# Optimization experiments

Measured on AMD Instinct MI355X. Metric: run time of the kernel, lower is better.

## Reference

```python
import jax, jax.numpy as jnp
import numpy as np

OBS, ACT, NTRAIN, BATCH = 8, 4, 128, 8
DIN = OBS + ACT


def setup_inputs() -> dict:
    key = jax.random.key(0)
    ks = jax.random.split(key, 11)
    f32 = jnp.float32
    m_x = jax.random.normal(ks[0], (BATCH, OBS), dtype=f32)
    A = 0.1 * jax.random.normal(ks[1], (BATCH, OBS, OBS), dtype=f32)
    s_x = A @ jnp.swapaxes(A, -1, -2) + 0.01 * jnp.eye(OBS, dtype=f32)  # SPD obs covariance
    m_u = jax.random.normal(ks[2], (BATCH, ACT), dtype=f32)
    Au = 0.1 * jax.random.normal(ks[3], (BATCH, ACT, ACT), dtype=f32)
    s_u = Au @ jnp.swapaxes(Au, -1, -2) + 0.01 * jnp.eye(ACT, dtype=f32)
    c_xu = 0.05 * jax.random.normal(ks[4], (BATCH, OBS, ACT), dtype=f32)
    X_train = jax.random.normal(ks[5], (NTRAIN, DIN), dtype=f32)
    lengthscales = jax.random.uniform(ks[6], (OBS, DIN), dtype=f32, minval=0.5, maxval=2.0)
    variances = jax.random.uniform(ks[7], (OBS, 1), dtype=f32, minval=0.5, maxval=1.5)
    noises = jax.random.uniform(ks[8], (OBS,), dtype=f32, minval=0.01, maxval=0.1)
    R = jax.random.normal(ks[9], (OBS, NTRAIN, NTRAIN), dtype=f32) / np.float32(np.sqrt(NTRAIN))
    inv_K = R @ jnp.swapaxes(R, -1, -2) + 0.1 * jnp.eye(NTRAIN, dtype=f32)  # SPD like a true K^-1
    beta = 0.1 * jax.random.normal(ks[10], (OBS, NTRAIN), dtype=f32)
    return dict(m_x=m_x, s_x=s_x, m_u=m_u, s_u=s_u, c_xu=c_xu, X_train=X_train,
                lengthscales=lengthscales, variances=variances, noises=noises,
                inv_K=inv_K, beta=beta)


def _forward(m_x, s_x, m_u, s_u, c_xu, X_train, lengthscales, variances, noises, inv_K, beta):
    obs_dim, input_dim = lengthscales.shape
    n = X_train.shape[0]
    eyeD = jnp.eye(input_dim, dtype=m_x.dtype)
    # joint input distribution over [x, u]
    joint_mean = jnp.concatenate([m_x, m_u], axis=-1)                      # [B, D]
    s_ = s_x @ c_xu                                                        # [B, obs, act] (as in source)
    upper = jnp.concatenate([s_x, s_], axis=-1)                            # [B, obs, D]
    lower = jnp.concatenate([jnp.swapaxes(s_, -1, -2), s_u], axis=-1)      # [B, act, D]
    joint_var = jnp.concatenate([upper, lower], axis=-2)                   # [B, D, D]
    # --- predictive mean (moment matching) ---
    inp = X_train[None, :, :] - joint_mean[:, None, :]                     # [B, N, D]
    inv_ls = 1.0 / lengthscales                                            # [E, D]
    inv_N = inp[:, None, :, :] * inv_ls[None, :, None, :]                  # [B, E, N, D]
    B_mat = inv_ls[None, :, :, None] * joint_var[:, None, :, :] * inv_ls[None, :, None, :] + eyeD
    t = jnp.swapaxes(jnp.linalg.solve(B_mat, jnp.swapaxes(inv_N, -1, -2)), -1, -2)  # [B, E, N, D]
    scaled_exp = jnp.exp(-0.5 * jnp.sum(inv_N * t, axis=-1))               # [B, E, N]
    lb = scaled_exp * beta[None, :, :]                                     # [B, E, N]
    det_B = jnp.linalg.det(B_mat)                                          # [B, E]
    var_v = variances[:, 0]                                                # [E]
    c = var_v[None, :] / jnp.sqrt(det_B)                                   # [B, E]
    pred_mean = jnp.sum(lb, axis=-1) * c                                   # [B, E]
    # --- input-output cross covariance ---
    t_inv_L = t * inv_ls[None, :, None, :]                                 # [B, E, N, D]
    cross_cov = jnp.swapaxes(jnp.einsum('bend,ben->bed', t_inv_L, lb) * c[..., None], -1, -2)  # [B, D, E]
    # --- predictive covariance: vectorized over all (a, b) output pairs ---
    X_i = X_train[:, None, :]
    X_j = X_train[None, :, :]
    diff = X_i - X_j                                                       # [N, N, D]
    l2 = lengthscales ** 2
    inv_l2 = 1.0 / l2

    def pair(l2_a, inv_a, var_a, beta_a, l2_b, inv_b, var_b, beta_b):
        inv_sum = inv_a + inv_b                                            # [D]
        Lam = 1.0 / inv_sum
        z_bar = Lam * (X_i * inv_a + X_j * inv_b)                          # [N, N, D]
        z = z_bar[None, :, :, :] - joint_mean[:, None, None, :]            # [B, N, N, D]
        z_flat = z.reshape(z.shape[0], n * n, input_dim)
        R_ab = joint_var * inv_sum[None, None, :] + eyeD                   # joint_var @ diag(inv_sum) + I
        exp1 = -0.5 * jnp.sum(diff * diff * (1.0 / (l2_a + l2_b)), axis=-1)  # [N, N]
        M_ab = joint_var + jnp.diag(Lam)[None, :, :]                       # [B, D, D]
        solved = jnp.swapaxes(jnp.linalg.solve(M_ab, jnp.swapaxes(z_flat, -1, -2)), -1, -2)
        exp2 = (-0.5 * jnp.sum(z_flat * solved, axis=-1)).reshape(z.shape[0], n, n)
        c_ab = var_a * var_b / jnp.sqrt(jnp.linalg.det(R_ab))              # [B]
        Q = c_ab[:, None, None] * jnp.exp(exp1[None, :, :] + exp2)         # [B, N, N]
        main = jnp.einsum('i,bij,j->b', beta_a, Q, beta_b)                 # [B]
        return main, Q

    pair_b = jax.vmap(pair, in_axes=(None, None, None, None, 0, 0, 0, 0))
    pair_ab = jax.vmap(pair_b, in_axes=(0, 0, 0, 0, None, None, None, None))
    main, Q = pair_ab(l2, inv_l2, var_v, beta, l2, inv_l2, var_v, beta)    # [E, E, B], [E, E, B, N, N]
    pred_cov = jnp.moveaxis(main, -1, 0)                                   # [B, E, E]
    idx = jnp.arange(obs_dim)
    Q_diag = Q[idx, idx]                                                   # [E, B, N, N]
    trace_val = jnp.einsum('eij,ebji->eb', inv_K, Q_diag)                  # [E, B]
    diag_corr = var_v[:, None] - trace_val + noises[:, None]               # [E, B]
    pred_cov = pred_cov + diag_corr.T[:, :, None] * jnp.eye(obs_dim, dtype=m_x.dtype)
    pred_cov = pred_cov - pred_mean[:, :, None] * pred_mean[:, None, :]
    pred_cov = 0.5 * (pred_cov + jnp.swapaxes(pred_cov, -1, -2))
    # --- propagate state moments ---
    cov_xf = upper @ cross_cov                                             # [B, obs, obs]
    m_out = m_x + pred_mean
    s_out = s_x + pred_cov + cov_xf + jnp.swapaxes(cov_xf, -1, -2)
    s_out = 0.5 * (s_out + jnp.swapaxes(s_out, -1, -2)) + 1e-8 * jnp.eye(obs_dim, dtype=m_x.dtype)
    return m_out, s_out


def reference(m_x, s_x, m_u, s_u, c_xu, X_train, lengthscales, variances, noises, inv_K, beta):
    return _forward(m_x, s_x, m_u, s_u, c_xu, X_train, lengthscales, variances, noises, inv_K, beta)
```

## Files before the change

kernel.cpp:

```cpp
#include <hip/hip_runtime.h>
#include <math.h>

#define OBS 8
#define ACT 4
#define DIN 12
#define NTRAIN 128
#define BATCH 8
#define NPAIR 36
#define NPT (BATCH*NPAIR)
#define NGT (BATCH*OBS)
#define NTASK (NPT+NGT)
#define THREADS 512
#define HSTRIDE 16

#define WS_PM  0
#define WS_CC  64
#define WS_MN  832
#define WS_TR  1344

__global__ void __launch_bounds__(THREADS) k_fused(
    const float* __restrict__ m_x, const float* __restrict__ s_x,
    const float* __restrict__ m_u, const float* __restrict__ s_u,
    const float* __restrict__ c_xu, const float* __restrict__ X,
    const float* __restrict__ ls, const float* __restrict__ vars,
    const float* __restrict__ beta, const float* __restrict__ invK,
    float* __restrict__ ws)
{
    int blk = blockIdx.x, tid = threadIdx.x;
    int lane = tid & 63, w = tid >> 6;
    bool isPair = blk < NPT;
    int b, a = 0, c = 0, e = 0;
    if (isPair) {
        b = blk / NPAIR;
        int rem = blk % NPAIR;
        while (rem >= OBS - a) { rem -= OBS - a; a++; }
        c = a + rem;
    } else {
        int q = blk - NPT; b = q / OBS; e = q % OBS;
    }

    __shared__ float jvs[144];
    __shared__ float Wl[144];
    __shared__ float mu[DIN];
    __shared__ float sc_wsum[DIN], sc_iA[DIN], sc_qc[DIN], sc_lam[DIN], sc_isum[DIN];
    __shared__ float s_cab;
    __shared__ __align__(16) float h[NTRAIN][HSTRIDE];
    __shared__ __align__(16) float2 bw[NTRAIN];
    __shared__ float red[8][13];

    int j0 = 2*lane;
    float xa[12], xb[12], xi[12];
    {
        const float4* xr = (const float4*)(X + j0*DIN);
        float4 t0 = xr[0], t1 = xr[1], t2 = xr[2], t3 = xr[3], t4 = xr[4], t5 = xr[5];
        xa[0]=t0.x; xa[1]=t0.y; xa[2]=t0.z; xa[3]=t0.w;
        xa[4]=t1.x; xa[5]=t1.y; xa[6]=t1.z; xa[7]=t1.w;
        xa[8]=t2.x; xa[9]=t2.y; xa[10]=t2.z; xa[11]=t2.w;
        xb[0]=t3.x; xb[1]=t3.y; xb[2]=t3.z; xb[3]=t3.w;
        xb[4]=t4.x; xb[5]=t4.y; xb[6]=t4.z; xb[7]=t4.w;
        xb[8]=t5.x; xb[9]=t5.y; xb[10]=t5.z; xb[11]=t5.w;
    }
    if (tid < NTRAIN) {
        const float4* xr = (const float4*)(X + tid*DIN);
        float4 t0 = xr[0], t1 = xr[1], t2 = xr[2];
        xi[0]=t0.x; xi[1]=t0.y; xi[2]=t0.z; xi[3]=t0.w;
        xi[4]=t1.x; xi[5]=t1.y; xi[6]=t1.z; xi[7]=t1.w;
        xi[8]=t2.x; xi[9]=t2.y; xi[10]=t2.z; xi[11]=t2.w;
    }

    if (tid < 144) {
        int r = tid / 12, cl = tid % 12;
        float v;
        if (r < OBS && cl < OBS) {
            v = s_x[(b*OBS+r)*OBS + cl];
        } else if (r < OBS) {
            v = 0.f;
            #pragma unroll
            for (int k = 0; k < OBS; k++)
                v += s_x[(b*OBS+r)*OBS+k] * c_xu[(b*OBS+k)*ACT + (cl-OBS)];
        } else if (cl < OBS) {
            v = 0.f;
            #pragma unroll
            for (int k = 0; k < OBS; k++)
                v += s_x[(b*OBS+cl)*OBS+k] * c_xu[(b*OBS+k)*ACT + (r-OBS)];
        } else {
            v = s_u[(b*ACT+r-OBS)*ACT + (cl-OBS)];
        }
        jvs[tid] = v;
    } else if (tid >= 160 && tid < 172) {
        int d = tid - 160;
        mu[d] = (d < OBS) ? m_x[b*OBS+d] : m_u[b*ACT+d-OBS];
    } else if (tid >= 192 && tid < 204) {
        int d = tid - 192;
        if (isPair) {
            float la = ls[a*DIN+d]; la *= la;
            float lc = ls[c*DIN+d]; lc *= lc;
            float ia = 1.f/la, ic = 1.f/lc;
            float is = ia + ic;
            float L  = 1.f/is;
            sc_wsum[d] = 1.f/(la+lc);
            sc_iA[d] = L*ia;
            sc_qc[d] = L*ic;
            sc_lam[d] = L;
            sc_isum[d] = is;
        } else {
            sc_iA[d] = 1.f / ls[e*DIN+d];
        }
    }
    __syncthreads();

    if (tid < DIN) {
        int r = tid;
        float row[12];
        if (isPair) {
            #pragma unroll
            for (int j = 0; j < 12; j++) row[j] = jvs[r*12+j];
            row[r] += sc_lam[r];
        } else {
            float ir = sc_iA[r];
            #pragma unroll
            for (int j = 0; j < 12; j++) row[j] = ir * sc_iA[j] * jvs[r*12+j];
            row[r] += 1.f;
        }
        float det = 1.f;
        #pragma unroll
        for (int k = 0; k < 12; k++) {
            float p = __shfl(row[k], k);
            float ip = 1.f / p;
            det *= p;
            float prow[12];
            #pragma unroll
            for (int j = 0; j < 12; j++) prow[j] = __shfl(row[j], k) * ip;
            if (r == k) {
                #pragma unroll
                for (int j = 0; j < 12; j++) row[j] = prow[j];
                row[k] = ip;
            } else {
                float f = row[k];
                #pragma unroll
                for (int j = 0; j < 12; j++) if (j != k) row[j] -= f * prow[j];
                row[k] = -f * ip;
            }
        }
        #pragma unroll
        for (int j = 0; j < 12; j++) Wl[r*12+j] = row[j];
        if (r == 0) {
            if (isPair) {
                float s = det;
                #pragma unroll
                for (int d = 0; d < 12; d++) s *= sc_isum[d];
                s_cab = vars[a]*vars[c] / sqrtf(s);
            } else {
                s_cab = vars[e] / sqrtf(det);
            }
        }
    }
    __syncthreads();

    if (isPair) {
        bool diag = (a == c);
        if (tid < NTRAIN) {
            int t = tid;
            float r[12], q[12]; float e1 = 0.f;
            #pragma unroll
            for (int d = 0; d < 12; d++) {
                r[d] = sc_iA[d]*xi[d] - mu[d];
                q[d] = sc_qc[d]*xi[d];
                e1 += sc_wsum[d]*xi[d]*xi[d];
            }
            float hrow[16];
            float alpha = 0.f, bq = 0.f;
            #pragma unroll
            for (int d = 0; d < 12; d++) {
                float u = 0.f, uq = 0.f;
                #pragma unroll
                for (int cl = 0; cl < 12; cl++) {
                    float wv = Wl[d*12+cl];
                    u  += wv*r[cl];
                    uq += wv*q[cl];
                }
                alpha += r[d]*u;
                bq    += q[d]*uq;
                hrow[d] = sc_wsum[d]*xi[d] - u*sc_qc[d];
            }
            hrow[12] = -0.5f*(e1 + alpha);
            hrow[13] = beta[a*NTRAIN+t];
            hrow[14] = 0.f; hrow[15] = 0.f;
            float4* hp = (float4*)&h[t][0];
            hp[0] = make_float4(hrow[0],hrow[1],hrow[2],hrow[3]);
            hp[1] = make_float4(hrow[4],hrow[5],hrow[6],hrow[7]);
            hp[2] = make_float4(hrow[8],hrow[9],hrow[10],hrow[11]);
            hp[3] = make_float4(hrow[12],hrow[13],hrow[14],hrow[15]);
            bw[t] = make_float2(-0.5f*(e1 + bq), beta[c*NTRAIN+t]);
        }
        __syncthreads();
        float4 bwv = ((const float4*)bw)[lane];
        float basej0 = bwv.x, wc0 = bwv.y, basej1 = bwv.z, wc1 = bwv.w;
        float am0 = 0.f, am1 = 0.f, at0 = 0.f, at1 = 0.f;
        const float2* Kb = (const float2*)(invK + a*NTRAIN*NTRAIN);
        #pragma unroll 4
        for (int k = 0; k < 16; k++) {
            int i = w + 8*k;
            const float4* hp = (const float4*)&h[i][0];
            float4 h0 = hp[0], h1 = hp[1], h2 = hp[2];
            float2 h3 = *(const float2*)&h[i][12];
            float sA0 = fmaf(h0.x,xa[0], fmaf(h0.y,xa[1], fmaf(h0.z,xa[2], h0.w*xa[3])));
            float sB0 = fmaf(h1.x,xa[4], fmaf(h1.y,xa[5], fmaf(h1.z,xa[6], h1.w*xa[7])));
            float sC0 = fmaf(h2.x,xa[8], fmaf(h2.y,xa[9], fmaf(h2.z,xa[10], h2.w*xa[11])));
            float sA1 = fmaf(h0.x,xb[0], fmaf(h0.y,xb[1], fmaf(h0.z,xb[2], h0.w*xb[3])));
            float sB1 = fmaf(h1.x,xb[4], fmaf(h1.y,xb[5], fmaf(h1.z,xb[6], h1.w*xb[7])));
            float sC1 = fmaf(h2.x,xb[8], fmaf(h2.y,xb[9], fmaf(h2.z,xb[10], h2.w*xb[11])));
            float e0  = __expf(sA0 + sB0 + sC0 + h3.x + basej0);
            float e1v = __expf(sA1 + sB1 + sC1 + h3.x + basej1);
            am0 = fmaf(h3.y, e0, am0);
            am1 = fmaf(h3.y, e1v, am1);
            if (diag) {
                float2 kv = Kb[i*64 + lane];
                at0 = fmaf(kv.x, e0, at0);
                at1 = fmaf(kv.y, e1v, at1);
            }
        }
        float accm = am0*wc0 + am1*wc1;
        float acct = at0 + at1;
        #pragma unroll
        for (int off = 32; off >= 1; off >>= 1) {
            accm += __shfl_xor(accm, off, 64);
            acct += __shfl_xor(acct, off, 64);
        }
        if (lane == 0) { red[w][0] = accm; red[w][1] = acct; }
        __syncthreads();
        if (tid == 0) {
            float m = 0.f, t = 0.f;
            #pragma unroll
            for (int v = 0; v < 8; v++) { m += red[v][0]; t += red[v][1]; }
            m *= s_cab; t *= s_cab;
            ws[WS_MN + b*64 + a*8 + c] = m;
            ws[WS_MN + b*64 + c*8 + a] = m;
            if (diag) ws[WS_TR + b*8 + a] = t;
        }
    } else {
        float vals[13];
        #pragma unroll
        for (int v = 0; v < 13; v++) vals[v] = 0.f;
        if (tid < NTRAIN) {
            int n = tid;
            float iN[12];
            #pragma unroll
            for (int d = 0; d < 12; d++) iN[d] = (xi[d]-mu[d]) * sc_iA[d];
            float qq = 0.f; float tv[12];
            #pragma unroll
            for (int d = 0; d < 12; d++) {
                float u = 0.f;
                #pragma unroll
                for (int cl = 0; cl < 12; cl++) u += Wl[d*12+cl]*iN[cl];
                tv[d] = u; qq += iN[d]*u;
            }
            float lb = __expf(-0.5f*qq) * beta[e*NTRAIN+n];
            vals[0] = lb;
            #pragma unroll
            for (int d = 0; d < 12; d++) vals[1+d] = tv[d]*sc_iA[d]*lb;
        }
        #pragma unroll
        for (int v = 0; v < 13; v++)
            #pragma unroll
            for (int off = 32; off >= 1; off >>= 1) vals[v] += __shfl_xor(vals[v], off, 64);
        if (lane == 0) {
            #pragma unroll
            for (int v = 0; v < 13; v++) red[w][v] = vals[v];
        }
        __syncthreads();
        if (tid == 0) {
            float cn = s_cab;
            ws[WS_PM + b*OBS + e] = cn*(red[0][0]+red[1][0]);
            for (int d = 0; d < 12; d++)
                ws[WS_CC + (b*DIN+d)*OBS + e] = cn*(red[0][1+d]+red[1][1+d]);
        }
    }
}

__global__ void k_final(const float* __restrict__ m_x, const float* __restrict__ s_x,
                        const float* __restrict__ c_xu, const float* __restrict__ vars,
                        const float* __restrict__ noises, const float* __restrict__ ws,
                        float* __restrict__ out) {
    int b = blockIdx.x, t = threadIdx.x;
    __shared__ float pm[OBS];
    __shared__ float sxs[64];
    const float* cc = ws + WS_CC + b*DIN*OBS;
    const float* mn = ws + WS_MN + b*64;
    const float* tr = ws + WS_TR + b*OBS;
    sxs[t] = s_x[b*64 + t];
    if (t < OBS) {
        float p = ws[WS_PM + b*OBS + t];
        pm[t] = p;
        out[b*OBS + t] = m_x[b*OBS + t] + p;
    }
    __syncthreads();
    int r = t >> 3, cl = t & 7;
    float P = mn[r*8 + cl];
    if (r == cl) P += vars[r] - tr[r] + noises[r];
    P -= pm[r]*pm[cl];
    float cxf = 0.f, cxfT = 0.f;
    #pragma unroll
    for (int d = 0; d < 8; d++) {
        cxf  += sxs[r*8+d]  * cc[d*8+cl];
        cxfT += sxs[cl*8+d] * cc[d*8+r];
    }
    #pragma unroll
    for (int d = 0; d < 4; d++) {
        float jr = 0.f, jc = 0.f;
        #pragma unroll
        for (int k = 0; k < 8; k++) {
            float cx = c_xu[(b*OBS+k)*ACT + d];
            jr += sxs[r*8+k]  * cx;
            jc += sxs[cl*8+k] * cx;
        }
        cxf  += jr * cc[(8+d)*8 + cl];
        cxfT += jc * cc[(8+d)*8 + r];
    }
    float S = sxs[r*8+cl] + P + cxf + cxfT;
    if (r == cl) S += 1e-8f;
    out[64 + b*64 + t] = S;
}

extern "C" void kernel_launch(void* const* d_in, const int* in_sizes, int n_in,
                              void* d_out, int out_size, void* d_ws, size_t ws_size,
                              hipStream_t stream) {
    const float* m_x    = (const float*)d_in[0];
    const float* s_x    = (const float*)d_in[1];
    const float* m_u    = (const float*)d_in[2];
    const float* s_u    = (const float*)d_in[3];
    const float* c_xu   = (const float*)d_in[4];
    const float* X      = (const float*)d_in[5];
    const float* ls     = (const float*)d_in[6];
    const float* vars   = (const float*)d_in[7];
    const float* noises = (const float*)d_in[8];
    const float* invK   = (const float*)d_in[9];
    const float* beta   = (const float*)d_in[10];
    float* out = (float*)d_out;
    float* ws  = (float*)d_ws;

    k_fused<<<NTASK, THREADS, 0, stream>>>(m_x, s_x, m_u, s_u, c_xu, X, ls, vars,
                                           beta, invK, ws);
    k_final<<<BATCH, 64, 0, stream>>>(m_x, s_x, c_xu, vars, noises, ws, out);
}
```

Baseline: 91.38 us.

## Merge GP-mean tasks into diagonal pair blocks and fuse final epilogue via last-block atomic

Folds the per-output GP mean/cross-covariance work into the diagonal pair blocks. It runs that work on threads 128-255 alongside the h-row setup, with both 12x12 inversions done in parallel in one wavefront. The separate finalization kernel is replaced by a last-block-done pattern: an atomic counter in the workspace, reset by a memset each launch, picks one block to compute the epilogue. This removes 64 extra blocks and one kernel launch, at the cost of an added memset, a device-wide atomic with fences, and a serialized tail in the last block.

```diff
diff --git a/kernel.cpp b/kernel.cpp
--- a/kernel.cpp
+++ b/kernel.cpp
@@ -7,9 +7,7 @@
 #define NTRAIN 128
 #define BATCH 8
 #define NPAIR 36
-#define NPT (BATCH*NPAIR)
-#define NGT (BATCH*OBS)
-#define NTASK (NPT+NGT)
+#define NBLK (BATCH*NPAIR)
 #define THREADS 512
 #define HSTRIDE 16
 
@@ -17,36 +15,37 @@
 #define WS_CC  64
 #define WS_MN  832
 #define WS_TR  1344
-
-__global__ void __launch_bounds__(THREADS) k_fused(
+#define WS_CNT 1536
+
+__global__ void __launch_bounds__(THREADS, 4) k_all(
     const float* __restrict__ m_x, const float* __restrict__ s_x,
     const float* __restrict__ m_u, const float* __restrict__ s_u,
     const float* __restrict__ c_xu, const float* __restrict__ X,
     const float* __restrict__ ls, const float* __restrict__ vars,
-    const float* __restrict__ beta, const float* __restrict__ invK,
-    float* __restrict__ ws)
+    const float* __restrict__ noises, const float* __restrict__ beta,
+    const float* __restrict__ invK, float* __restrict__ ws,
+    float* __restrict__ out)
 {
     int blk = blockIdx.x, tid = threadIdx.x;
     int lane = tid & 63, w = tid >> 6;
-    bool isPair = blk < NPT;
-    int b, a = 0, c = 0, e = 0;
-    if (isPair) {
-        b = blk / NPAIR;
-        int rem = blk % NPAIR;
-        while (rem >= OBS - a) { rem -= OBS - a; a++; }
-        c = a + rem;
-    } else {
-        int q = blk - NPT; b = q / OBS; e = q % OBS;
-    }
+    int b = blk / NPAIR;
+    int rem = blk % NPAIR;
+    int a = 0;
+    while (rem >= OBS - a) { rem -= OBS - a; a++; }
+    int c = a + rem;
+    bool diag = (a == c);
 
     __shared__ float jvs[144];
     __shared__ float Wl[144];
+    __shared__ float Wg[144];
     __shared__ float mu[DIN];
-    __shared__ float sc_wsum[DIN], sc_iA[DIN], sc_qc[DIN], sc_lam[DIN], sc_isum[DIN];
-    __shared__ float s_cab;
+    __shared__ float sc_wsum[DIN], sc_iA[DIN], sc_qc[DIN], sc_lam[DIN], sc_isum[DIN], sc_il[DIN];
+    __shared__ float s_cab, s_cgp;
     __shared__ __align__(16) float h[NTRAIN][HSTRIDE];
     __shared__ __align__(16) float2 bw[NTRAIN];
     __shared__ float red[8][13];
+    __shared__ float redg[2][16];
+    __shared__ unsigned int s_last;
 
     int j0 = 2*lane;
     float xa[12], xb[12], xi[12];
@@ -60,8 +59,9 @@
         xb[4]=t4.x; xb[5]=t4.y; xb[6]=t4.z; xb[7]=t4.w;
         xb[8]=t5.x; xb[9]=t5.y; xb[10]=t5.z; xb[11]=t5.w;
     }
-    if (tid < NTRAIN) {
-        const float4* xr = (const float4*)(X + tid*DIN);
+    if (tid < 256) {
+        int rowi = tid & 127;
+        const float4* xr = (const float4*)(X + rowi*DIN);
         float4 t0 = xr[0], t1 = xr[1], t2 = xr[2];
         xi[0]=t0.x; xi[1]=t0.y; xi[2]=t0.z; xi[3]=t0.w;
         xi[4]=t1.x; xi[5]=t1.y; xi[6]=t1.z; xi[7]=t1.w;
@@ -92,45 +92,47 @@
         mu[d] = (d < OBS) ? m_x[b*OBS+d] : m_u[b*ACT+d-OBS];
     } else if (tid >= 192 && tid < 204) {
         int d = tid - 192;
-        if (isPair) {
-            float la = ls[a*DIN+d]; la *= la;
-            float lc = ls[c*DIN+d]; lc *= lc;
-            float ia = 1.f/la, ic = 1.f/lc;
-            float is = ia + ic;
-            float L  = 1.f/is;
-            sc_wsum[d] = 1.f/(la+lc);
-            sc_iA[d] = L*ia;
-            sc_qc[d] = L*ic;
-            sc_lam[d] = L;
-            sc_isum[d] = is;
+        float la = ls[a*DIN+d]; la *= la;
+        float lc = ls[c*DIN+d]; lc *= lc;
+        float ia = 1.f/la, ic = 1.f/lc;
+        float is = ia + ic;
+        float L  = 1.f/is;
+        sc_wsum[d] = 1.f/(la+lc);
+        sc_iA[d] = L*ia;
+        sc_qc[d] = L*ic;
+        sc_lam[d] = L;
+        sc_isum[d] = is;
+    } else if (tid >= 224 && tid < 236) {
+        int d = tid - 224;
+        sc_il[d] = 1.f / ls[a*DIN+d];
+    }
+    __syncthreads();
+
+    if (tid < 64 && lane < 28) {
+        int grp = lane >> 4;
+        int base = grp << 4;
+        int r = lane - base;
+        int rr = (r < 12) ? r : 0;
+        float row[12];
+        if (grp == 0) {
+            #pragma unroll
+            for (int j = 0; j < 12; j++) row[j] = jvs[rr*12+j];
+            row[rr] += sc_lam[rr];
         } else {
-            sc_iA[d] = 1.f / ls[e*DIN+d];
-        }
-    }
-    __syncthreads();
-
-    if (tid < DIN) {
-        int r = tid;
-        float row[12];
-        if (isPair) {
-            #pragma unroll
-            for (int j = 0; j < 12; j++) row[j] = jvs[r*12+j];
-            row[r] += sc_lam[r];
-        } else {
-            float ir = sc_iA[r];
-            #pragma unroll
-            for (int j = 0; j < 12; j++) row[j] = ir * sc_iA[j] * jvs[r*12+j];
+            float ir = sc_il[r];
+            #pragma unroll
+            for (int j = 0; j < 12; j++) row[j] = ir * sc_il[j] * jvs[r*12+j];
             row[r] += 1.f;
         }
         float det = 1.f;
         #pragma unroll
         for (int k = 0; k < 12; k++) {
-            float p = __shfl(row[k], k);
+            float p = __shfl(row[k], base + k);
             float ip = 1.f / p;
             det *= p;
             float prow[12];
             #pragma unroll
-            for (int j = 0; j < 12; j++) prow[j] = __shfl(row[j], k) * ip;
+            for (int j = 0; j < 12; j++) prow[j] = __shfl(row[j], base + k) * ip;
             if (r == k) {
                 #pragma unroll
                 for (int j = 0; j < 12; j++) row[j] = prow[j];
@@ -142,184 +144,184 @@
                 row[k] = -f * ip;
             }
         }
-        #pragma unroll
-        for (int j = 0; j < 12; j++) Wl[r*12+j] = row[j];
-        if (r == 0) {
-            if (isPair) {
-                float s = det;
-                #pragma unroll
-                for (int d = 0; d < 12; d++) s *= sc_isum[d];
-                s_cab = vars[a]*vars[c] / sqrtf(s);
-            } else {
-                s_cab = vars[e] / sqrtf(det);
+        if (r < 12) {
+            float* W = grp ? Wg : Wl;
+            #pragma unroll
+            for (int j = 0; j < 12; j++) W[r*12+j] = row[j];
+        }
+        if (lane == 0) {
+            float s = det;
+            #pragma unroll
+            for (int d = 0; d < 12; d++) s *= sc_isum[d];
+            s_cab = vars[a]*vars[c] / sqrtf(s);
+        }
+        if (lane == 16) s_cgp = vars[a] / sqrtf(det);
+    }
+    __syncthreads();
+
+    if (tid < NTRAIN) {
+        int t = tid;
+        float r[12], q[12]; float e1 = 0.f;
+        #pragma unroll
+        for (int d = 0; d < 12; d++) {
+            r[d] = sc_iA[d]*xi[d] - mu[d];
+            q[d] = sc_qc[d]*xi[d];
+            e1 += sc_wsum[d]*xi[d]*xi[d];
+        }
+        float hrow[16];
+        float alpha = 0.f, bq = 0.f;
+        #pragma unroll
+        for (int d = 0; d < 12; d++) {
+            float u = 0.f, uq = 0.f;
+            #pragma unroll
+            for (int cl = 0; cl < 12; cl++) {
+                float wv = Wl[d*12+cl];
+                u  += wv*r[cl];
+                uq += wv*q[cl];
             }
-        }
-    }
-    __syncthreads();
-
-    if (isPair) {
-        bool diag = (a == c);
-        if (tid < NTRAIN) {
-            int t = tid;
-            float r[12], q[12]; float e1 = 0.f;
-            #pragma unroll
-            for (int d = 0; d < 12; d++) {
-                r[d] = sc_iA[d]*xi[d] - mu[d];
-                q[d] = sc_qc[d]*xi[d];
-                e1 += sc_wsum[d]*xi[d]*xi[d];
-            }
-            float hrow[16];
-            float alpha = 0.f, bq = 0.f;
-            #pragma unroll
-            for (int d = 0; d < 12; d++) {
-                float u = 0.f, uq = 0.f;
-                #pragma unroll
-                for (int cl = 0; cl < 12; cl++) {
-                    float wv = Wl[d*12+cl];
-                    u  += wv*r[cl];
-                    uq += wv*q[cl];
-                }
-                alpha += r[d]*u;
-                bq    += q[d]*uq;
-                hrow[d] = sc_wsum[d]*xi[d] - u*sc_qc[d];
-            }
-            hrow[12] = -0.5f*(e1 + alpha);
-            hrow[13] = beta[a*NTRAIN+t];
-            hrow[14] = 0.f; hrow[15] = 0.f;
-            float4* hp = (float4*)&h[t][0];
-            hp[0] = make_float4(hrow[0],hrow[1],hrow[2],hrow[3]);
-            hp[1] = make_float4(hrow[4],hrow[5],hrow[6],hrow[7]);
-            hp[2] = make_float4(hrow[8],hrow[9],hrow[10],hrow[11]);
-            hp[3] = make_float4(hrow[12],hrow[13],hrow[14],hrow[15]);
-            bw[t] = make_float2(-0.5f*(e1 + bq), beta[c*NTRAIN+t]);
-        }
-        __syncthreads();
-        float4 bwv = ((const float4*)bw)[lane];
-        float basej0 = bwv.x, wc0 = bwv.y, basej1 = bwv.z, wc1 = bwv.w;
-        float am0 = 0.f, am1 = 0.f, at0 = 0.f, at1 = 0.f;
-        const float2* Kb = (const float2*)(invK + a*NTRAIN*NTRAIN);
-        #pragma unroll 4
-        for (int k = 0; k < 16; k++) {
-            int i = w + 8*k;
-            const float4* hp = (const float4*)&h[i][0];
-            float4 h0 = hp[0], h1 = hp[1], h2 = hp[2];
-            float2 h3 = *(const float2*)&h[i][12];
-            float sA0 = fmaf(h0.x,xa[0], fmaf(h0.y,xa[1], fmaf(h0.z,xa[2], h0.w*xa[3])));
-            float sB0 = fmaf(h1.x,xa[4], fmaf(h1.y,xa[5], fmaf(h1.z,xa[6], h1.w*xa[7])));
-            float sC0 = fmaf(h2.x,xa[8], fmaf(h2.y,xa[9], fmaf(h2.z,xa[10], h2.w*xa[11])));
-            float sA1 = fmaf(h0.x,xb[0], fmaf(h0.y,xb[1], fmaf(h0.z,xb[2], h0.w*xb[3])));
-            float sB1 = fmaf(h1.x,xb[4], fmaf(h1.y,xb[5], fmaf(h1.z,xb[6], h1.w*xb[7])));
-            float sC1 = fmaf(h2.x,xb[8], fmaf(h2.y,xb[9], fmaf(h2.z,xb[10], h2.w*xb[11])));
-            float e0  = __expf(sA0 + sB0 + sC0 + h3.x + basej0);
-            float e1v = __expf(sA1 + sB1 + sC1 + h3.x + basej1);
-            am0 = fmaf(h3.y, e0, am0);
-            am1 = fmaf(h3.y, e1v, am1);
-            if (diag) {
-                float2 kv = Kb[i*64 + lane];
-                at0 = fmaf(kv.x, e0, at0);
-                at1 = fmaf(kv.y, e1v, at1);
-            }
-        }
-        float accm = am0*wc0 + am1*wc1;
-        float acct = at0 + at1;
-        #pragma unroll
-        for (int off = 32; off >= 1; off >>= 1) {
-            accm += __shfl_xor(accm, off, 64);
-            acct += __shfl_xor(acct, off, 64);
-        }
-        if (lane == 0) { red[w][0] = accm; red[w][1] = acct; }
-        __syncthreads();
-        if (tid == 0) {
-            float m = 0.f, t = 0.f;
-            #pragma unroll
-            for (int v = 0; v < 8; v++) { m += red[v][0]; t += red[v][1]; }
-            m *= s_cab; t *= s_cab;
-            ws[WS_MN + b*64 + a*8 + c] = m;
-            ws[WS_MN + b*64 + c*8 + a] = m;
-            if (diag) ws[WS_TR + b*8 + a] = t;
-        }
-    } else {
+            alpha += r[d]*u;
+            bq    += q[d]*uq;
+            hrow[d] = sc_wsum[d]*xi[d] - u*sc_qc[d];
+        }
+        hrow[12] = -0.5f*(e1 + alpha);
+        hrow[13] = beta[a*NTRAIN+t];
+        hrow[14] = 0.f; hrow[15] = 0.f;
+        float4* hp = (float4*)&h[t][0];
+        hp[0] = make_float4(hrow[0],hrow[1],hrow[2],hrow[3]);
+        hp[1] = make_float4(hrow[4],hrow[5],hrow[6],hrow[7]);
+        hp[2] = make_float4(hrow[8],hrow[9],hrow[10],hrow[11]);
+        hp[3] = make_float4(hrow[12],hrow[13],hrow[14],hrow[15]);
+        bw[t] = make_float2(-0.5f*(e1 + bq), beta[c*NTRAIN+t]);
+    } else if (diag && tid < 256) {
+        int n = tid - 128;
+        float iN[12], tv[12];
+        #pragma unroll
+        for (int d = 0; d < 12; d++) iN[d] = (xi[d] - mu[d]) * sc_il[d];
+        float qq = 0.f;
+        #pragma unroll
+        for (int d = 0; d < 12; d++) {
+            float u = 0.f;
+            #pragma unroll
+            for (int cl = 0; cl < 12; cl++) u += Wg[d*12+cl]*iN[cl];
+            tv[d] = u; qq += iN[d]*u;
+        }
+        float lb = __expf(-0.5f*qq) * beta[a*NTRAIN+n];
         float vals[13];
-        #pragma unroll
-        for (int v = 0; v < 13; v++) vals[v] = 0.f;
-        if (tid < NTRAIN) {
-            int n = tid;
-            float iN[12];
-            #pragma unroll
-            for (int d = 0; d < 12; d++) iN[d] = (xi[d]-mu[d]) * sc_iA[d];
-            float qq = 0.f; float tv[12];
-            #pragma unroll
-            for (int d = 0; d < 12; d++) {
-                float u = 0.f;
-                #pragma unroll
-                for (int cl = 0; cl < 12; cl++) u += Wl[d*12+cl]*iN[cl];
-                tv[d] = u; qq += iN[d]*u;
-            }
-            float lb = __expf(-0.5f*qq) * beta[e*NTRAIN+n];
-            vals[0] = lb;
-            #pragma unroll
-            for (int d = 0; d < 12; d++) vals[1+d] = tv[d]*sc_iA[d]*lb;
-        }
+        vals[0] = lb;
+        #pragma unroll
+        for (int d = 0; d < 12; d++) vals[1+d] = tv[d]*sc_il[d]*lb;
         #pragma unroll
         for (int v = 0; v < 13; v++)
             #pragma unroll
             for (int off = 32; off >= 1; off >>= 1) vals[v] += __shfl_xor(vals[v], off, 64);
         if (lane == 0) {
             #pragma unroll
-            for (int v = 0; v < 13; v++) red[w][v] = vals[v];
-        }
+            for (int v = 0; v < 13; v++) redg[w-2][v] = vals[v];
+        }
+    }
+    __syncthreads();
+
+    float4 bwv = ((const float4*)bw)[lane];
+    float basej0 = bwv.x, wc0 = bwv.y, basej1 = bwv.z, wc1 = bwv.w;
+    float am0 = 0.f, am1 = 0.f, at0 = 0.f, at1 = 0.f;
+    const float2* Kb = (const float2*)(invK + a*NTRAIN*NTRAIN);
+    #pragma unroll 4
+    for (int k = 0; k < 16; k++) {
+        int i = w + 8*k;
+        const float4* hp = (const float4*)&h[i][0];
+        float4 h0 = hp[0], h1 = hp[1], h2 = hp[2];
+        float2 h3 = *(const float2*)&h[i][12];
+        float sA0 = fmaf(h0.x,xa[0], fmaf(h0.y,xa[1], fmaf(h0.z,xa[2], h0.w*xa[3])));
+        float sB0 = fmaf(h1.x,xa[4], fmaf(h1.y,xa[5], fmaf(h1.z,xa[6], h1.w*xa[7])));
+        float sC0 = fmaf(h2.x,xa[8], fmaf(h2.y,xa[9], fmaf(h2.z,xa[10], h2.w*xa[11])));
+        float sA1 = fmaf(h0.x,xb[0], fmaf(h0.y,xb[1], fmaf(h0.z,xb[2], h0.w*xb[3])));
+        float sB1 = fmaf(h1.x,xb[4], fmaf(h1.y,xb[5], fmaf(h1.z,xb[6], h1.w*xb[7])));
+        float sC1 = fmaf(h2.x,xb[8], fmaf(h2.y,xb[9], fmaf(h2.z,xb[10], h2.w*xb[11])));
+        float e0  = __expf(sA0 + sB0 + sC0 + h3.x + basej0);
+        float e1v = __expf(sA1 + sB1 + sC1 + h3.x + basej1);
+        am0 = fmaf(h3.y, e0, am0);
+        am1 = fmaf(h3.y, e1v, am1);
+        if (diag) {
+            float2 kv = Kb[i*64 + lane];
+            at0 = fmaf(kv.x, e0, at0);
+            at1 = fmaf(kv.y, e1v, at1);
+        }
+    }
+    float accm = am0*wc0 + am1*wc1;
+    float acct = at0 + at1;
+    #pragma unroll
+    for (int off = 32; off >= 1; off >>= 1) {
+        accm += __shfl_xor(accm, off, 64);
+        acct += __shfl_xor(acct, off, 64);
+    }
+    if (lane == 0) { red[w][0] = accm; red[w][1] = acct; }
+    __syncthreads();
+    if (tid == 0) {
+        float m = 0.f, t = 0.f;
+        #pragma unroll
+        for (int v = 0; v < 8; v++) { m += red[v][0]; t += red[v][1]; }
+        m *= s_cab; t *= s_cab;
+        ws[WS_MN + b*64 + a*8 + c] = m;
+        ws[WS_MN + b*64 + c*8 + a] = m;
+        if (diag) ws[WS_TR + b*8 + a] = t;
+    } else if (tid == 64 && diag) {
+        float cn = s_cgp;
+        ws[WS_PM + b*OBS + a] = cn*(redg[0][0]+redg[1][0]);
+        #pragma unroll
+        for (int d = 0; d < 12; d++)
+            ws[WS_CC + (b*DIN+d)*OBS + a] = cn*(redg[0][1+d]+redg[1][1+d]);
+    }
+    __syncthreads();
+
+    if (tid == 0) {
+        __threadfence();
+        unsigned int old = __hip_atomic_fetch_add(
+            (unsigned int*)(ws + WS_CNT), 1u,
+            __ATOMIC_ACQ_REL, __HIP_MEMORY_SCOPE_AGENT);
+        s_last = (old == NBLK - 1) ? 1u : 0u;
+    }
+    __syncthreads();
+
+    if (s_last) {
+        __threadfence();
+        float* epiSx = &h[0][0];
+        float* epiPm = &h[64][0];
+        epiSx[tid] = s_x[tid];
+        if (tid < 64) epiPm[tid] = ws[WS_PM + tid];
         __syncthreads();
-        if (tid == 0) {
-            float cn = s_cab;
-            ws[WS_PM + b*OBS + e] = cn*(red[0][0]+red[1][0]);
-            for (int d = 0; d < 12; d++)
-                ws[WS_CC + (b*DIN+d)*OBS + e] = cn*(red[0][1+d]+red[1][1+d]);
-        }
-    }
-}
-
-__global__ void k_final(const float* __restrict__ m_x, const float* __restrict__ s_x,
-                        const float* __restrict__ c_xu, const float* __restrict__ vars,
-                        const float* __restrict__ noises, const float* __restrict__ ws,
-                        float* __restrict__ out) {
-    int b = blockIdx.x, t = threadIdx.x;
-    __shared__ float pm[OBS];
-    __shared__ float sxs[64];
-    const float* cc = ws + WS_CC + b*DIN*OBS;
-    const float* mn = ws + WS_MN + b*64;
-    const float* tr = ws + WS_TR + b*OBS;
-    sxs[t] = s_x[b*64 + t];
-    if (t < OBS) {
-        float p = ws[WS_PM + b*OBS + t];
-        pm[t] = p;
-        out[b*OBS + t] = m_x[b*OBS + t] + p;
-    }
-    __syncthreads();
-    int r = t >> 3, cl = t & 7;
-    float P = mn[r*8 + cl];
-    if (r == cl) P += vars[r] - tr[r] + noises[r];
-    P -= pm[r]*pm[cl];
-    float cxf = 0.f, cxfT = 0.f;
-    #pragma unroll
-    for (int d = 0; d < 8; d++) {
-        cxf  += sxs[r*8+d]  * cc[d*8+cl];
-        cxfT += sxs[cl*8+d] * cc[d*8+r];
-    }
-    #pragma unroll
-    for (int d = 0; d < 4; d++) {
-        float jr = 0.f, jc = 0.f;
-        #pragma unroll
-        for (int k = 0; k < 8; k++) {
-            float cx = c_xu[(b*OBS+k)*ACT + d];
-            jr += sxs[r*8+k]  * cx;
-            jc += sxs[cl*8+k] * cx;
-        }
-        cxf  += jr * cc[(8+d)*8 + cl];
-        cxfT += jc * cc[(8+d)*8 + r];
-    }
-    float S = sxs[r*8+cl] + P + cxf + cxfT;
-    if (r == cl) S += 1e-8f;
-    out[64 + b*64 + t] = S;
+        int bb = w, t = lane;
+        int r = t >> 3, cl = t & 7;
+        const float* cc  = ws + WS_CC + bb*DIN*OBS;
+        const float* mn  = ws + WS_MN + bb*64;
+        const float* tr  = ws + WS_TR + bb*OBS;
+        const float* sxs = epiSx + bb*64;
+        const float* pm8 = epiPm + bb*8;
+        float P = mn[r*8 + cl];
+        if (r == cl) P += vars[r] - tr[r] + noises[r];
+        P -= pm8[r]*pm8[cl];
+        float cxf = 0.f, cxfT = 0.f;
+        #pragma unroll
+        for (int d = 0; d < 8; d++) {
+            cxf  += sxs[r*8+d]  * cc[d*8+cl];
+            cxfT += sxs[cl*8+d] * cc[d*8+r];
+        }
+        #pragma unroll
+        for (int d = 0; d < 4; d++) {
+            float jr = 0.f, jc = 0.f;
+            #pragma unroll
+            for (int k = 0; k < 8; k++) {
+                float cx = c_xu[(bb*OBS+k)*ACT + d];
+                jr += sxs[r*8+k]  * cx;
+                jc += sxs[cl*8+k] * cx;
+            }
+            cxf  += jr * cc[(8+d)*8 + cl];
+            cxfT += jc * cc[(8+d)*8 + r];
+        }
+        float S = sxs[r*8+cl] + P + cxf + cxfT;
+        if (r == cl) S += 1e-8f;
+        out[64 + bb*64 + t] = S;
+        if (t < OBS) out[bb*OBS + t] = m_x[bb*OBS + t] + pm8[t];
+    }
 }
 
 extern "C" void kernel_launch(void* const* d_in, const int* in_sizes, int n_in,
@@ -339,7 +341,7 @@
     float* out = (float*)d_out;
     float* ws  = (float*)d_ws;
 
-    k_fused<<<NTASK, THREADS, 0, stream>>>(m_x, s_x, m_u, s_u, c_xu, X, ls, vars,
-                                           beta, invK, ws);
-    k_final<<<BATCH, 64, 0, stream>>>(m_x, s_x, c_xu, vars, noises, ws, out);
+    hipMemsetAsync((char*)d_ws + WS_CNT*sizeof(float), 0, 4, stream);
+    k_all<<<NBLK, THREADS, 0, stream>>>(m_x, s_x, m_u, s_u, c_xu, X, ls, vars,
+                                        noises, beta, invK, ws, out);
 }
```

Result: slower. 106.6 us (+16.7%).
